# Kernel tuning notes

Hardware: AMD Instinct MI355X
Metric: run time of the kernel (lower is better)

Reference implementation:

```python
import jax, jax.numpy as jnp
import numpy as np

C, H, W = 16, 512, 512
HID = 128
N_STEPS = 8


def setup_inputs() -> dict:
    key = jax.random.key(0)
    k1, k2, k3 = jax.random.split(key, 3)
    state = jax.random.normal(k1, (C, H, W), dtype=jnp.float32)
    # MLP params: 5*C = 80 gathered features -> HID -> C delta channels
    W1 = jax.random.normal(k2, (5 * C, HID), dtype=jnp.float32) * (1.0 / np.sqrt(5 * C))
    b1 = jnp.zeros((HID,), dtype=jnp.float32)
    W2 = jax.random.normal(k3, (HID, C), dtype=jnp.float32) * (1.0 / np.sqrt(HID))
    b2 = jnp.zeros((C,), dtype=jnp.float32)
    return {"state": state, "W1": W1, "b1": b1, "W2": W2, "b2": b2, "n_steps": N_STEPS}


def _neighbor_idx(n):
    i = jnp.arange(n)
    minus = jnp.maximum(i - 1, 0)          # clamp at low edge (cy==0 -> 0)
    plus = jnp.where(i == n - 1, 0, i + 1)  # WRAP to 0 at high edge (original quirk)
    return minus, plus


def reference(state, W1, b1, W2, b2, n_steps):
    c, h, w = state.shape
    up, down = _neighbor_idx(h)
    left, right = _neighbor_idx(w)

    def step(s, _):
        # von-Neumann gather: (5C, H, W), feature order [center, up, down, left, right]
        feats = jnp.concatenate(
            [s, s[:, up, :], s[:, down, :], s[:, :, left], s[:, :, right]], axis=0)
        x = feats.reshape(5 * c, h * w).T        # (HW, 5C)
        hdn = jax.nn.relu(x @ W1 + b1)           # (HW, HID)
        delta = (hdn @ W2 + b2).T.reshape(c, h, w)
        s_new = s + delta
        s_new = s_new.at[0].set(s[0])            # channel 0 snapshot restore
        return s_new, None

    out, _ = jax.lax.scan(step, state, None, length=n_steps)
    return out
```

## Files before the change

### kernel.cpp

```cpp
#include <hip/hip_runtime.h>
#include <hip/hip_bf16.h>

#define HH 512
#define WW 512
#define CC 16
#define HIDN 128
#define HWSZ (HH*WW)

typedef __attribute__((ext_vector_type(8))) short short8;
typedef __attribute__((ext_vector_type(4))) short short4v;
typedef __attribute__((ext_vector_type(4))) float float4v;

__device__ __forceinline__ short to_bf16(float f){
    __hip_bfloat16 h = __float2bfloat16(f);
    return __builtin_bit_cast(short, h);
}

__global__ void __launch_bounds__(256) prep_kernel(
    const float* __restrict__ W1, const float* __restrict__ W2,
    short* __restrict__ w1t, short* __restrict__ w2t)
{
    int t = blockIdx.x * blockDim.x + threadIdx.x;
    int stride = gridDim.x * blockDim.x;
    for (int idx = t; idx < HIDN*96; idx += stride){
        int n = idx / 96;
        int k = idx - n*96;
        float v = (k < 80) ? W1[k*HIDN + n] : 0.0f;
        w1t[idx] = to_bf16(v);
    }
    for (int idx = t; idx < CC*HIDN; idx += stride){
        int n = idx >> 7;
        int k = idx & 127;
        w2t[idx] = to_bf16(W2[k*CC + n]);
    }
}

#define RSTRIDE 24
#define RROW    (68*RSTRIDE)

__global__ void __launch_bounds__(256, 5) step_kernel(
    const float* __restrict__ src, float* __restrict__ dst,
    const short* __restrict__ w1t, const short* __restrict__ w2t,
    const float* __restrict__ b1, const float* __restrict__ b2)
{
    __shared__ __align__(16) short rows_u[3*RROW];
    __shared__ __align__(16) short hdn[64][136];

    const int t    = threadIdx.x;
    const int w    = t >> 6;
    const int lane = t & 63;
    const int ln15 = lane & 15;
    const int g4   = lane >> 4;

    const int bx = blockIdx.x;
    const int y  = bx >> 3;
    const int xs = (bx & 7) << 6;

    const int yu = (y == 0)      ? 0 : (y - 1);
    const int yd = (y == HH - 1) ? 0 : (y + 1);

    if (t < 192){
        const int r  = t >> 6;
        const int l  = t & 63;
        const int q  = l & 15;
        const int cq = l >> 4;
        const int rowg = (r == 0) ? y : ((r == 1) ? yu : yd);
        const float* base = src + (size_t)rowg * WW + xs + (q << 2);
        float4v f[4];
        #pragma unroll
        for (int i = 0; i < 4; ++i)
            f[i] = *(const float4v*)(base + (size_t)((cq << 2) + i) * HWSZ);
        #pragma unroll
        for (int j = 0; j < 4; ++j){
            short4v v;
            v[0] = to_bf16(f[0][j]); v[1] = to_bf16(f[1][j]);
            v[2] = to_bf16(f[2][j]); v[3] = to_bf16(f[3][j]);
            *(short4v*)&rows_u[r*RROW + ((q << 2) + 1 + j)*RSTRIDE + (cq << 2)] = v;
        }
    } else if (t < 224){
        const int c    = (t - 192) & 15;
        const int side = (t - 192) >> 4;
        const int gx   = (side == 0) ? ((xs == 0) ? 0 : xs - 1)
                                     : ((xs + 64 == WW) ? 0 : xs + 64);
        rows_u[(side * 65)*RSTRIDE + c] =
            to_bf16(src[(size_t)c*HWSZ + (size_t)y*WW + gx]);
    }

    int offB[3];
    #pragma unroll
    for (int kk = 0; kk < 3; ++kk){
        const int g  = (kk < 2) ? ((kk << 2) + g4) : (8 + (g4 & 1));
        const int n  = g >> 1;
        const int cb = (g & 1) << 3;
        const int r  = (n == 1) ? 1 : ((n == 2) ? 2 : 0);
        const int dx = (n == 3) ? -1 : ((n == 4) ? 1 : 0);
        offB[kk] = r*RROW + (ln15 + 1 + dx)*RSTRIDE + cb;
    }

    __syncthreads();

    float4v acc[2][4];
    #pragma unroll
    for (int mt = 0; mt < 2; ++mt)
        #pragma unroll
        for (int nt = 0; nt < 4; ++nt)
            acc[mt][nt] = (float4v){0.f, 0.f, 0.f, 0.f};

    #pragma unroll
    for (int kk = 0; kk < 3; ++kk){
        short8 bfragF[4];
        #pragma unroll
        for (int nt = 0; nt < 4; ++nt)
            bfragF[nt] = *(const short8*)(&rows_u[offB[kk] + nt * (16 * RSTRIDE)]);
        #pragma unroll
        for (int mt = 0; mt < 2; ++mt){
            const int hrow = (((w << 1) + mt) << 4) + ln15;
            short8 afragW = *(const short8*)(w1t + hrow * 96 + (kk << 5) + (g4 << 3));
            #pragma unroll
            for (int nt = 0; nt < 4; ++nt)
                acc[mt][nt] = __builtin_amdgcn_mfma_f32_16x16x32_bf16(
                    afragW, bfragF[nt], acc[mt][nt], 0, 0, 0);
        }
    }

    #pragma unroll
    for (int mt = 0; mt < 2; ++mt){
        const int hbase = (((w << 1) + mt) << 4) + (g4 << 2);
        const float4v bb = *(const float4v*)(b1 + hbase);
        #pragma unroll
        for (int nt = 0; nt < 4; ++nt){
            short4v s;
            #pragma unroll
            for (int r = 0; r < 4; ++r){
                float v = acc[mt][nt][r] + bb[r];
                v = v > 0.f ? v : 0.f;
                s[r] = to_bf16(v);
            }
            *(short4v*)&hdn[(nt << 4) + ln15][hbase] = s;
        }
    }
    __syncthreads();

    const int pxb = (w << 4) + (g4 << 2);
    const size_t gofs = (size_t)ln15 * HWSZ + (size_t)y * WW + xs + pxb;
    const float4v sold = *(const float4v*)(src + gofs);
    const float bias2 = b2[ln15];

    float4v acc2 = (float4v){0.f, 0.f, 0.f, 0.f};
    #pragma unroll
    for (int kk = 0; kk < 4; ++kk){
        const int k0 = kk << 5;
        short8 a = *(const short8*)(&hdn[(w << 4) + ln15][k0 + (g4 << 3)]);
        short8 b = *(const short8*)(w2t + ln15 * HIDN + k0 + (g4 << 3));
        acc2 = __builtin_amdgcn_mfma_f32_16x16x32_bf16(a, b, acc2, 0, 0, 0);
    }

    float4v outv;
    #pragma unroll
    for (int r = 0; r < 4; ++r){
        const float v = sold[r] + acc2[r] + bias2;
        outv[r] = (ln15 == 0) ? sold[r] : v;
    }
    *(float4v*)(dst + gofs) = outv;
}

extern "C" void kernel_launch(void* const* d_in, const int* in_sizes, int n_in,
                              void* d_out, int out_size, void* d_ws, size_t ws_size,
                              hipStream_t stream)
{
    const float* state = (const float*)d_in[0];
    const float* W1    = (const float*)d_in[1];
    const float* b1    = (const float*)d_in[2];
    const float* W2    = (const float*)d_in[3];
    const float* b2    = (const float*)d_in[4];

    float* B1  = (float*)d_ws;
    short* w1t = (short*)((char*)d_ws + (size_t)HWSZ * CC * 4);
    short* w2t = w1t + HIDN * 96;
    float* out = (float*)d_out;

    prep_kernel<<<32, 256, 0, stream>>>(W1, W2, w1t, w2t);

    dim3 grid(HH * (WW / 64));
    step_kernel<<<grid, 256, 0, stream>>>(state, B1, w1t, w2t, b1, b2);
    step_kernel<<<grid, 256, 0, stream>>>(B1, out, w1t, w2t, b1, b2);
    step_kernel<<<grid, 256, 0, stream>>>(out, B1, w1t, w2t, b1, b2);
    step_kernel<<<grid, 256, 0, stream>>>(B1, out, w1t, w2t, b1, b2);
    step_kernel<<<grid, 256, 0, stream>>>(out, B1, w1t, w2t, b1, b2);
    step_kernel<<<grid, 256, 0, stream>>>(B1, out, w1t, w2t, b1, b2);
    step_kernel<<<grid, 256, 0, stream>>>(out, B1, w1t, w2t, b1, b2);
    step_kernel<<<grid, 256, 0, stream>>>(B1, out, w1t, w2t, b1, b2);
}
```

Baseline: 264.2 us.

## Fuse eight step launches into one persistent cooperative kernel with grid sync

Replaces the eight per-step kernel launches with a single cooperative kernel of 1024 blocks. Each block processes four strips per step, and a grid-wide barrier separates consecutive steps, which removes launch gaps and per-launch tail effects. If the cooperative launch fails, it falls back to the original eight launches. The trade-off is grid-sync overhead, a lower occupancy bound (4 blocks per SM instead of 5), and a missing __syncthreads between strips that reuse the same shared buffers, which risks a race.

```diff
diff --git a/kernel.cpp b/kernel.cpp
--- a/kernel.cpp
+++ b/kernel.cpp
@@ -1,5 +1,8 @@
 #include <hip/hip_runtime.h>
 #include <hip/hip_bf16.h>
+#include <hip/hip_cooperative_groups.h>
+
+namespace cg = cooperative_groups;
 
 #define HH 512
 #define WW 512
@@ -38,24 +41,13 @@
 #define RSTRIDE 24
 #define RROW    (68*RSTRIDE)
 
-__global__ void __launch_bounds__(256, 5) step_kernel(
+__device__ __forceinline__ void do_strip(
     const float* __restrict__ src, float* __restrict__ dst,
     const short* __restrict__ w1t, const short* __restrict__ w2t,
-    const float* __restrict__ b1, const float* __restrict__ b2)
-{
-    __shared__ __align__(16) short rows_u[3*RROW];
-    __shared__ __align__(16) short hdn[64][136];
-
-    const int t    = threadIdx.x;
-    const int w    = t >> 6;
-    const int lane = t & 63;
-    const int ln15 = lane & 15;
-    const int g4   = lane >> 4;
-
-    const int bx = blockIdx.x;
-    const int y  = bx >> 3;
-    const int xs = (bx & 7) << 6;
-
+    const float* __restrict__ b1, const float bias2,
+    short* __restrict__ rows_u, short (*hdn)[136], const int* offB,
+    int t, int w, int ln15, int g4, int y, int xs)
+{
     const int yu = (y == 0)      ? 0 : (y - 1);
     const int yd = (y == HH - 1) ? 0 : (y + 1);
 
@@ -85,18 +77,6 @@
         rows_u[(side * 65)*RSTRIDE + c] =
             to_bf16(src[(size_t)c*HWSZ + (size_t)y*WW + gx]);
     }
-
-    int offB[3];
-    #pragma unroll
-    for (int kk = 0; kk < 3; ++kk){
-        const int g  = (kk < 2) ? ((kk << 2) + g4) : (8 + (g4 & 1));
-        const int n  = g >> 1;
-        const int cb = (g & 1) << 3;
-        const int r  = (n == 1) ? 1 : ((n == 2) ? 2 : 0);
-        const int dx = (n == 3) ? -1 : ((n == 4) ? 1 : 0);
-        offB[kk] = r*RROW + (ln15 + 1 + dx)*RSTRIDE + cb;
-    }
-
     __syncthreads();
 
     float4v acc[2][4];
@@ -144,7 +124,6 @@
     const int pxb = (w << 4) + (g4 << 2);
     const size_t gofs = (size_t)ln15 * HWSZ + (size_t)y * WW + xs + pxb;
     const float4v sold = *(const float4v*)(src + gofs);
-    const float bias2 = b2[ln15];
 
     float4v acc2 = (float4v){0.f, 0.f, 0.f, 0.f};
     #pragma unroll
@@ -164,15 +143,95 @@
     *(float4v*)(dst + gofs) = outv;
 }
 
+__global__ void __launch_bounds__(256, 4) fused_kernel(
+    const float* __restrict__ state, float* __restrict__ B1, float* __restrict__ out,
+    const short* __restrict__ w1t, const short* __restrict__ w2t,
+    const float* __restrict__ b1, const float* __restrict__ b2)
+{
+    cg::grid_group gg = cg::this_grid();
+
+    __shared__ __align__(16) short rows_u[3*RROW];
+    __shared__ __align__(16) short hdn[64][136];
+
+    const int t    = threadIdx.x;
+    const int w    = t >> 6;
+    const int lane = t & 63;
+    const int ln15 = lane & 15;
+    const int g4   = lane >> 4;
+    const int b    = blockIdx.x;
+
+    int offB[3];
+    #pragma unroll
+    for (int kk = 0; kk < 3; ++kk){
+        const int g  = (kk < 2) ? ((kk << 2) + g4) : (8 + (g4 & 1));
+        const int n  = g >> 1;
+        const int cb = (g & 1) << 3;
+        const int r  = (n == 1) ? 1 : ((n == 2) ? 2 : 0);
+        const int dx = (n == 3) ? -1 : ((n == 4) ? 1 : 0);
+        offB[kk] = r*RROW + (ln15 + 1 + dx)*RSTRIDE + cb;
+    }
+    const float bias2 = b2[ln15];
+
+    #pragma unroll 1
+    for (int step = 0; step < 8; ++step){
+        const float* src = (step == 0) ? state : ((step & 1) ? B1 : out);
+        float* dst = (step & 1) ? out : B1;
+
+        #pragma unroll 1
+        for (int i = 0; i < 4; ++i){
+            const int s  = b + (i << 10);
+            const int y  = s >> 3;
+            const int xs = (s & 7) << 6;
+            do_strip(src, dst, w1t, w2t, b1, bias2,
+                     rows_u, hdn, offB, t, w, ln15, g4, y, xs);
+        }
+        if (step < 7) gg.sync();
+    }
+}
+
+__global__ void __launch_bounds__(256, 5) step_kernel(
+    const float* __restrict__ src, float* __restrict__ dst,
+    const short* __restrict__ w1t, const short* __restrict__ w2t,
+    const float* __restrict__ b1, const float* __restrict__ b2)
+{
+    __shared__ __align__(16) short rows_u[3*RROW];
+    __shared__ __align__(16) short hdn[64][136];
+
+    const int t    = threadIdx.x;
+    const int w    = t >> 6;
+    const int lane = t & 63;
+    const int ln15 = lane & 15;
+    const int g4   = lane >> 4;
+
+    const int bx = blockIdx.x;
+    const int y  = bx >> 3;
+    const int xs = (bx & 7) << 6;
+
+    int offB[3];
+    #pragma unroll
+    for (int kk = 0; kk < 3; ++kk){
+        const int g  = (kk < 2) ? ((kk << 2) + g4) : (8 + (g4 & 1));
+        const int n  = g >> 1;
+        const int cb = (g & 1) << 3;
+        const int r  = (n == 1) ? 1 : ((n == 2) ? 2 : 0);
+        const int dx = (n == 3) ? -1 : ((n == 4) ? 1 : 0);
+        offB[kk] = r*RROW + (ln15 + 1 + dx)*RSTRIDE + cb;
+    }
+    const float bias2 = b2[ln15];
+
+    do_strip(src, dst, w1t, w2t, b1, bias2,
+             rows_u, hdn, offB, t, w, ln15, g4, y, xs);
+}
+
 extern "C" void kernel_launch(void* const* d_in, const int* in_sizes, int n_in,
                               void* d_out, int out_size, void* d_ws, size_t ws_size,
                               hipStream_t stream)
 {
     const float* state = (const float*)d_in[0];
     const float* W1    = (const float*)d_in[1];
-    const float* b1    = (const float*)d_in[2];
+    const float* b1p   = (const float*)d_in[2];
     const float* W2    = (const float*)d_in[3];
-    const float* b2    = (const float*)d_in[4];
+    const float* b2p   = (const float*)d_in[4];
 
     float* B1  = (float*)d_ws;
     short* w1t = (short*)((char*)d_ws + (size_t)HWSZ * CC * 4);
@@ -181,13 +240,23 @@
 
     prep_kernel<<<32, 256, 0, stream>>>(W1, W2, w1t, w2t);
 
-    dim3 grid(HH * (WW / 64));
-    step_kernel<<<grid, 256, 0, stream>>>(state, B1, w1t, w2t, b1, b2);
-    step_kernel<<<grid, 256, 0, stream>>>(B1, out, w1t, w2t, b1, b2);
-    step_kernel<<<grid, 256, 0, stream>>>(out, B1, w1t, w2t, b1, b2);
-    step_kernel<<<grid, 256, 0, stream>>>(B1, out, w1t, w2t, b1, b2);
-    step_kernel<<<grid, 256, 0, stream>>>(out, B1, w1t, w2t, b1, b2);
-    step_kernel<<<grid, 256, 0, stream>>>(B1, out, w1t, w2t, b1, b2);
-    step_kernel<<<grid, 256, 0, stream>>>(out, B1, w1t, w2t, b1, b2);
-    step_kernel<<<grid, 256, 0, stream>>>(B1, out, w1t, w2t, b1, b2);
-}
+    void* kargs[] = {
+        (void*)&state, (void*)&B1, (void*)&out,
+        (void*)&w1t, (void*)&w2t, (void*)&b1p, (void*)&b2p
+    };
+    hipError_t err = hipLaunchCooperativeKernel(
+        (const void*)fused_kernel, dim3(1024), dim3(256), kargs, 0, stream);
+
+    if (err != hipSuccess){
+        (void)hipGetLastError();
+        dim3 grid(HH * (WW / 64));
+        step_kernel<<<grid, 256, 0, stream>>>(state, B1, w1t, w2t, b1p, b2p);
+        step_kernel<<<grid, 256, 0, stream>>>(B1, out, w1t, w2t, b1p, b2p);
+        step_kernel<<<grid, 256, 0, stream>>>(out, B1, w1t, w2t, b1p, b2p);
+        step_kernel<<<grid, 256, 0, stream>>>(B1, out, w1t, w2t, b1p, b2p);
+        step_kernel<<<grid, 256, 0, stream>>>(out, B1, w1t, w2t, b1p, b2p);
+        step_kernel<<<grid, 256, 0, stream>>>(B1, out, w1t, w2t, b1p, b2p);
+        step_kernel<<<grid, 256, 0, stream>>>(out, B1, w1t, w2t, b1p, b2p);
+        step_kernel<<<grid, 256, 0, stream>>>(B1, out, w1t, w2t, b1p, b2p);
+    }
+}
```

Measured after the change: 1.025 ms. 288% more time.

## Fuse two automaton steps per kernel with halo recomputation of neighbor rows

Applied to the files above, without the earlier changes.

Each kernel launch now performs two update steps. The block recomputes the first step for its own row and the rows above and below (plus a 1-pixel column halo) into shared memory, then computes the second step from those values. This halves the number of launches and global round-trips of the state, at the cost of roughly three times the first-step MLP work, more shared memory and lower occupancy.

```diff
diff --git a/kernel.cpp b/kernel.cpp
--- a/kernel.cpp
+++ b/kernel.cpp
@@ -10,6 +10,7 @@
 typedef __attribute__((ext_vector_type(8))) short short8;
 typedef __attribute__((ext_vector_type(4))) short short4v;
 typedef __attribute__((ext_vector_type(4))) float float4v;
+typedef __attribute__((ext_vector_type(2))) float float2v;
 
 __device__ __forceinline__ short to_bf16(float f){
     __hip_bfloat16 h = __float2bfloat16(f);
@@ -38,13 +39,15 @@
 #define RSTRIDE 24
 #define RROW    (68*RSTRIDE)
 
-__global__ void __launch_bounds__(256, 5) step_kernel(
+__global__ void __launch_bounds__(256, 4) step2_kernel(
     const float* __restrict__ src, float* __restrict__ dst,
     const short* __restrict__ w1t, const short* __restrict__ w2t,
     const float* __restrict__ b1, const float* __restrict__ b2)
 {
+    __shared__ __align__(16) short rows_s[3*RROW];
     __shared__ __align__(16) short rows_u[3*RROW];
-    __shared__ __align__(16) short hdn[64][136];
+    __shared__ __align__(16) short hdn[66][136];
+    float* ctr = (float*)rows_s;
 
     const int t    = threadIdx.x;
     const int w    = t >> 6;
@@ -59,34 +62,7 @@
     const int yu = (y == 0)      ? 0 : (y - 1);
     const int yd = (y == HH - 1) ? 0 : (y + 1);
 
-    if (t < 192){
-        const int r  = t >> 6;
-        const int l  = t & 63;
-        const int q  = l & 15;
-        const int cq = l >> 4;
-        const int rowg = (r == 0) ? y : ((r == 1) ? yu : yd);
-        const float* base = src + (size_t)rowg * WW + xs + (q << 2);
-        float4v f[4];
-        #pragma unroll
-        for (int i = 0; i < 4; ++i)
-            f[i] = *(const float4v*)(base + (size_t)((cq << 2) + i) * HWSZ);
-        #pragma unroll
-        for (int j = 0; j < 4; ++j){
-            short4v v;
-            v[0] = to_bf16(f[0][j]); v[1] = to_bf16(f[1][j]);
-            v[2] = to_bf16(f[2][j]); v[3] = to_bf16(f[3][j]);
-            *(short4v*)&rows_u[r*RROW + ((q << 2) + 1 + j)*RSTRIDE + (cq << 2)] = v;
-        }
-    } else if (t < 224){
-        const int c    = (t - 192) & 15;
-        const int side = (t - 192) >> 4;
-        const int gx   = (side == 0) ? ((xs == 0) ? 0 : xs - 1)
-                                     : ((xs + 64 == WW) ? 0 : xs + 64);
-        rows_u[(side * 65)*RSTRIDE + c] =
-            to_bf16(src[(size_t)c*HWSZ + (size_t)y*WW + gx]);
-    }
-
-    int offB[3];
+    int offA[3];
     #pragma unroll
     for (int kk = 0; kk < 3; ++kk){
         const int g  = (kk < 2) ? ((kk << 2) + g4) : (8 + (g4 & 1));
@@ -94,74 +70,199 @@
         const int cb = (g & 1) << 3;
         const int r  = (n == 1) ? 1 : ((n == 2) ? 2 : 0);
         const int dx = (n == 3) ? -1 : ((n == 4) ? 1 : 0);
-        offB[kk] = r*RROW + (ln15 + 1 + dx)*RSTRIDE + cb;
-    }
-
+        offA[kk] = r*RROW + (ln15 + 1 + dx)*RSTRIDE + cb;
+    }
+    const float bias2 = b2[ln15];
+
+    const int excA = (xs == 0   && ln15 == 0) ? RSTRIDE : 0;
+    const int excB = (xs == 448 && ln15 == 1 && g4 >= 2) ? RSTRIDE : 0;
+
+    #pragma unroll 1
+    for (int pass = 0; pass < 3; ++pass){
+        const int slot = (pass == 0) ? 1 : ((pass == 1) ? 2 : 0);
+        const int gr   = (pass == 0) ? yu : ((pass == 1) ? yd : y);
+
+        if (t < 204){
+            const int r3 = (t >= 136) ? 2 : ((t >= 68) ? 1 : 0);
+            const int u  = t - r3 * 68;
+            const int q  = u >> 2;
+            const int cq = u & 3;
+            const int rowg = (r3 == 0) ? gr
+                           : ((r3 == 1) ? ((gr == 0) ? 0 : gr - 1)
+                                        : ((gr == HH - 1) ? 0 : gr + 1));
+            const int c0 = xs - 2 + (q << 2);
+            float4v f[4];
+            if (c0 >= 0 && c0 <= 508){
+                const float* base = src + (size_t)rowg * WW + c0;
+                #pragma unroll
+                for (int i = 0; i < 4; ++i){
+                    const float* p = base + (size_t)((cq << 2) + i) * HWSZ;
+                    float2v lo = *(const float2v*)(p);
+                    float2v hi = *(const float2v*)(p + 2);
+                    f[i][0] = lo[0]; f[i][1] = lo[1]; f[i][2] = hi[0]; f[i][3] = hi[1];
+                }
+            } else {
+                #pragma unroll
+                for (int j = 0; j < 4; ++j){
+                    int c = c0 + j;
+                    c = (c < 0) ? 0 : ((c >= 512) ? c - 512 : c);
+                    #pragma unroll
+                    for (int i = 0; i < 4; ++i)
+                        f[i][j] = src[(size_t)((cq << 2) + i) * HWSZ + (size_t)rowg * WW + c];
+                }
+            }
+            #pragma unroll
+            for (int j = 0; j < 4; ++j){
+                short4v v;
+                v[0] = to_bf16(f[0][j]); v[1] = to_bf16(f[1][j]);
+                v[2] = to_bf16(f[2][j]); v[3] = to_bf16(f[3][j]);
+                *(short4v*)&rows_s[r3*RROW + ((q << 2) + j)*RSTRIDE + (cq << 2)] = v;
+            }
+        }
+        __syncthreads();
+
+        float4v acc[2][5];
+        #pragma unroll
+        for (int mt = 0; mt < 2; ++mt)
+            #pragma unroll
+            for (int nt = 0; nt < 5; ++nt)
+                acc[mt][nt] = (float4v){0.f, 0.f, 0.f, 0.f};
+
+        #pragma unroll
+        for (int kk = 0; kk < 3; ++kk){
+            short8 bfragF[5];
+            #pragma unroll
+            for (int nt = 0; nt < 5; ++nt){
+                int ao = offA[kk] + nt * (16 * RSTRIDE);
+                if (kk == 2 && nt == 0) ao += excA;
+                if (kk == 1 && nt == 4) ao += excB;
+                bfragF[nt] = *(const short8*)(&rows_s[ao]);
+            }
+            #pragma unroll
+            for (int mt = 0; mt < 2; ++mt){
+                const int hrow = (((w << 1) + mt) << 4) + ln15;
+                short8 afragW = *(const short8*)(w1t + hrow * 96 + (kk << 5) + (g4 << 3));
+                #pragma unroll
+                for (int nt = 0; nt < 5; ++nt)
+                    acc[mt][nt] = __builtin_amdgcn_mfma_f32_16x16x32_bf16(
+                        afragW, bfragF[nt], acc[mt][nt], 0, 0, 0);
+            }
+        }
+
+        #pragma unroll
+        for (int mt = 0; mt < 2; ++mt){
+            const int hbase = (((w << 1) + mt) << 4) + (g4 << 2);
+            const float4v bb = *(const float4v*)(b1 + hbase);
+            #pragma unroll
+            for (int nt = 0; nt < 5; ++nt){
+                if (nt == 4 && ln15 >= 2) continue;
+                short4v s;
+                #pragma unroll
+                for (int r = 0; r < 4; ++r){
+                    float v = acc[mt][nt][r] + bb[r];
+                    v = v > 0.f ? v : 0.f;
+                    s[r] = to_bf16(v);
+                }
+                *(short4v*)&hdn[(nt << 4) + ln15][hbase] = s;
+            }
+        }
+        __syncthreads();
+
+        #pragma unroll 1
+        for (int tile = w; tile < 5; tile += 4){
+            const int arow = (tile < 4) ? ((tile << 4) + ln15) : (64 + (ln15 & 1));
+            float4v a2 = (float4v){0.f, 0.f, 0.f, 0.f};
+            #pragma unroll
+            for (int kk = 0; kk < 4; ++kk){
+                const int k0 = kk << 5;
+                short8 a = *(const short8*)(&hdn[arow][k0 + (g4 << 3)]);
+                short8 b = *(const short8*)(w2t + ln15 * HIDN + k0 + (g4 << 3));
+                a2 = __builtin_amdgcn_mfma_f32_16x16x32_bf16(a, b, a2, 0, 0, 0);
+            }
+            const int pb = (tile << 4) + (g4 << 2);
+            #pragma unroll
+            for (int r = 0; r < 4; ++r){
+                const int p = pb + r;
+                int c = xs - 1 + p;
+                c = (c < 0) ? 0 : ((c >= 512) ? c - 512 : c);
+                const float sold = src[(size_t)ln15 * HWSZ + (size_t)gr * WW + c];
+                const float val = (ln15 == 0) ? sold : (sold + a2[r] + bias2);
+                if (p <= 65){
+                    rows_u[slot * RROW + p * RSTRIDE + ln15] = to_bf16(val);
+                    if (slot == 0 && p >= 1 && p <= 64)
+                        ctr[((p - 1) << 4) + ln15] = val;
+                }
+            }
+        }
+    }
     __syncthreads();
 
-    float4v acc[2][4];
-    #pragma unroll
-    for (int mt = 0; mt < 2; ++mt)
-        #pragma unroll
-        for (int nt = 0; nt < 4; ++nt)
-            acc[mt][nt] = (float4v){0.f, 0.f, 0.f, 0.f};
-
-    #pragma unroll
-    for (int kk = 0; kk < 3; ++kk){
-        short8 bfragF[4];
-        #pragma unroll
-        for (int nt = 0; nt < 4; ++nt)
-            bfragF[nt] = *(const short8*)(&rows_u[offB[kk] + nt * (16 * RSTRIDE)]);
+    {
+        float4v acc[2][4];
+        #pragma unroll
+        for (int mt = 0; mt < 2; ++mt)
+            #pragma unroll
+            for (int nt = 0; nt < 4; ++nt)
+                acc[mt][nt] = (float4v){0.f, 0.f, 0.f, 0.f};
+
+        #pragma unroll
+        for (int kk = 0; kk < 3; ++kk){
+            short8 bfragF[4];
+            #pragma unroll
+            for (int nt = 0; nt < 4; ++nt)
+                bfragF[nt] = *(const short8*)(&rows_u[offA[kk] + nt * (16 * RSTRIDE)]);
+            #pragma unroll
+            for (int mt = 0; mt < 2; ++mt){
+                const int hrow = (((w << 1) + mt) << 4) + ln15;
+                short8 afragW = *(const short8*)(w1t + hrow * 96 + (kk << 5) + (g4 << 3));
+                #pragma unroll
+                for (int nt = 0; nt < 4; ++nt)
+                    acc[mt][nt] = __builtin_amdgcn_mfma_f32_16x16x32_bf16(
+                        afragW, bfragF[nt], acc[mt][nt], 0, 0, 0);
+            }
+        }
+
         #pragma unroll
         for (int mt = 0; mt < 2; ++mt){
-            const int hrow = (((w << 1) + mt) << 4) + ln15;
-            short8 afragW = *(const short8*)(w1t + hrow * 96 + (kk << 5) + (g4 << 3));
-            #pragma unroll
-            for (int nt = 0; nt < 4; ++nt)
-                acc[mt][nt] = __builtin_amdgcn_mfma_f32_16x16x32_bf16(
-                    afragW, bfragF[nt], acc[mt][nt], 0, 0, 0);
-        }
-    }
-
-    #pragma unroll
-    for (int mt = 0; mt < 2; ++mt){
-        const int hbase = (((w << 1) + mt) << 4) + (g4 << 2);
-        const float4v bb = *(const float4v*)(b1 + hbase);
-        #pragma unroll
-        for (int nt = 0; nt < 4; ++nt){
-            short4v s;
-            #pragma unroll
-            for (int r = 0; r < 4; ++r){
-                float v = acc[mt][nt][r] + bb[r];
-                v = v > 0.f ? v : 0.f;
-                s[r] = to_bf16(v);
-            }
-            *(short4v*)&hdn[(nt << 4) + ln15][hbase] = s;
+            const int hbase = (((w << 1) + mt) << 4) + (g4 << 2);
+            const float4v bb = *(const float4v*)(b1 + hbase);
+            #pragma unroll
+            for (int nt = 0; nt < 4; ++nt){
+                short4v s;
+                #pragma unroll
+                for (int r = 0; r < 4; ++r){
+                    float v = acc[mt][nt][r] + bb[r];
+                    v = v > 0.f ? v : 0.f;
+                    s[r] = to_bf16(v);
+                }
+                *(short4v*)&hdn[(nt << 4) + ln15][hbase] = s;
+            }
         }
     }
     __syncthreads();
 
-    const int pxb = (w << 4) + (g4 << 2);
-    const size_t gofs = (size_t)ln15 * HWSZ + (size_t)y * WW + xs + pxb;
-    const float4v sold = *(const float4v*)(src + gofs);
-    const float bias2 = b2[ln15];
-
-    float4v acc2 = (float4v){0.f, 0.f, 0.f, 0.f};
-    #pragma unroll
-    for (int kk = 0; kk < 4; ++kk){
-        const int k0 = kk << 5;
-        short8 a = *(const short8*)(&hdn[(w << 4) + ln15][k0 + (g4 << 3)]);
-        short8 b = *(const short8*)(w2t + ln15 * HIDN + k0 + (g4 << 3));
-        acc2 = __builtin_amdgcn_mfma_f32_16x16x32_bf16(a, b, acc2, 0, 0, 0);
-    }
-
-    float4v outv;
-    #pragma unroll
-    for (int r = 0; r < 4; ++r){
-        const float v = sold[r] + acc2[r] + bias2;
-        outv[r] = (ln15 == 0) ? sold[r] : v;
-    }
-    *(float4v*)(dst + gofs) = outv;
+    {
+        const int pxb = (w << 4) + (g4 << 2);
+        const size_t gofs = (size_t)ln15 * HWSZ + (size_t)y * WW + xs + pxb;
+
+        float4v a2 = (float4v){0.f, 0.f, 0.f, 0.f};
+        #pragma unroll
+        for (int kk = 0; kk < 4; ++kk){
+            const int k0 = kk << 5;
+            short8 a = *(const short8*)(&hdn[(w << 4) + ln15][k0 + (g4 << 3)]);
+            short8 b = *(const short8*)(w2t + ln15 * HIDN + k0 + (g4 << 3));
+            a2 = __builtin_amdgcn_mfma_f32_16x16x32_bf16(a, b, a2, 0, 0, 0);
+        }
+
+        float4v outv;
+        #pragma unroll
+        for (int r = 0; r < 4; ++r){
+            const float sold = ctr[((pxb + r) << 4) + ln15];
+            const float v = sold + a2[r] + bias2;
+            outv[r] = (ln15 == 0) ? sold : v;
+        }
+        *(float4v*)(dst + gofs) = outv;
+    }
 }
 
 extern "C" void kernel_launch(void* const* d_in, const int* in_sizes, int n_in,
@@ -170,9 +271,9 @@
 {
     const float* state = (const float*)d_in[0];
     const float* W1    = (const float*)d_in[1];
-    const float* b1    = (const float*)d_in[2];
+    const float* b1p   = (const float*)d_in[2];
     const float* W2    = (const float*)d_in[3];
-    const float* b2    = (const float*)d_in[4];
+    const float* b2p   = (const float*)d_in[4];
 
     float* B1  = (float*)d_ws;
     short* w1t = (short*)((char*)d_ws + (size_t)HWSZ * CC * 4);
@@ -182,12 +283,8 @@
     prep_kernel<<<32, 256, 0, stream>>>(W1, W2, w1t, w2t);
 
     dim3 grid(HH * (WW / 64));
-    step_kernel<<<grid, 256, 0, stream>>>(state, B1, w1t, w2t, b1, b2);
-    step_kernel<<<grid, 256, 0, stream>>>(B1, out, w1t, w2t, b1, b2);
-    step_kernel<<<grid, 256, 0, stream>>>(out, B1, w1t, w2t, b1, b2);
-    step_kernel<<<grid, 256, 0, stream>>>(B1, out, w1t, w2t, b1, b2);
-    step_kernel<<<grid, 256, 0, stream>>>(out, B1, w1t, w2t, b1, b2);
-    step_kernel<<<grid, 256, 0, stream>>>(B1, out, w1t, w2t, b1, b2);
-    step_kernel<<<grid, 256, 0, stream>>>(out, B1, w1t, w2t, b1, b2);
-    step_kernel<<<grid, 256, 0, stream>>>(B1, out, w1t, w2t, b1, b2);
-}
+    step2_kernel<<<grid, 256, 0, stream>>>(state, B1, w1t, w2t, b1p, b2p);
+    step2_kernel<<<grid, 256, 0, stream>>>(B1, out, w1t, w2t, b1p, b2p);
+    step2_kernel<<<grid, 256, 0, stream>>>(out, B1, w1t, w2t, b1p, b2p);
+    step2_kernel<<<grid, 256, 0, stream>>>(B1, out, w1t, w2t, b1p, b2p);
+}
```

After: 559.0 us. 112% more time.

## Process four tiles per block with register prefetch of next tile

Applied to the files above, without the earlier changes.

Each block now handles four consecutive 64-pixel tiles along a row instead of one. The grid shrinks from 4096 to 1024 blocks, and block indices are remapped so blocks are interleaved across rows. The next tile's global loads are issued into registers before the current tile's MFMA work, so load latency overlaps compute. The aim is to cut per-block launch and setup overhead and hide memory latency. The cost is fewer blocks, which lowers available parallelism, and extra live registers for the prefetch.

```diff
diff --git a/kernel.cpp b/kernel.cpp
--- a/kernel.cpp
+++ b/kernel.cpp
@@ -38,27 +38,10 @@
 #define RSTRIDE 24
 #define RROW    (68*RSTRIDE)
 
-__global__ void __launch_bounds__(256, 5) step_kernel(
-    const float* __restrict__ src, float* __restrict__ dst,
-    const short* __restrict__ w1t, const short* __restrict__ w2t,
-    const float* __restrict__ b1, const float* __restrict__ b2)
-{
-    __shared__ __align__(16) short rows_u[3*RROW];
-    __shared__ __align__(16) short hdn[64][136];
-
-    const int t    = threadIdx.x;
-    const int w    = t >> 6;
-    const int lane = t & 63;
-    const int ln15 = lane & 15;
-    const int g4   = lane >> 4;
-
-    const int bx = blockIdx.x;
-    const int y  = bx >> 3;
-    const int xs = (bx & 7) << 6;
-
-    const int yu = (y == 0)      ? 0 : (y - 1);
-    const int yd = (y == HH - 1) ? 0 : (y + 1);
-
+__device__ __forceinline__ void stage_load(
+    const float* __restrict__ src, int t, int y, int yu, int yd, int xs,
+    float4v f[4], float* halo)
+{
     if (t < 192){
         const int r  = t >> 6;
         const int l  = t & 63;
@@ -66,10 +49,26 @@
         const int cq = l >> 4;
         const int rowg = (r == 0) ? y : ((r == 1) ? yu : yd);
         const float* base = src + (size_t)rowg * WW + xs + (q << 2);
-        float4v f[4];
         #pragma unroll
         for (int i = 0; i < 4; ++i)
             f[i] = *(const float4v*)(base + (size_t)((cq << 2) + i) * HWSZ);
+    } else if (t < 224){
+        const int c    = (t - 192) & 15;
+        const int side = (t - 192) >> 4;
+        const int gx   = (side == 0) ? ((xs == 0) ? 0 : xs - 1)
+                                     : ((xs + 64 == WW) ? 0 : xs + 64);
+        *halo = src[(size_t)c * HWSZ + (size_t)y * WW + gx];
+    }
+}
+
+__device__ __forceinline__ void stage_write(
+    short* __restrict__ rows_u, int t, const float4v f[4], float halo)
+{
+    if (t < 192){
+        const int r  = t >> 6;
+        const int l  = t & 63;
+        const int q  = l & 15;
+        const int cq = l >> 4;
         #pragma unroll
         for (int j = 0; j < 4; ++j){
             short4v v;
@@ -80,11 +79,31 @@
     } else if (t < 224){
         const int c    = (t - 192) & 15;
         const int side = (t - 192) >> 4;
-        const int gx   = (side == 0) ? ((xs == 0) ? 0 : xs - 1)
-                                     : ((xs + 64 == WW) ? 0 : xs + 64);
-        rows_u[(side * 65)*RSTRIDE + c] =
-            to_bf16(src[(size_t)c*HWSZ + (size_t)y*WW + gx]);
-    }
+        rows_u[(side * 65)*RSTRIDE + c] = to_bf16(halo);
+    }
+}
+
+__global__ void __launch_bounds__(256, 5) step_kernel(
+    const float* __restrict__ src, float* __restrict__ dst,
+    const short* __restrict__ w1t, const short* __restrict__ w2t,
+    const float* __restrict__ b1, const float* __restrict__ b2)
+{
+    __shared__ __align__(16) short rows_u[3*RROW];
+    __shared__ __align__(16) short hdn[64][136];
+
+    const int t    = threadIdx.x;
+    const int w    = t >> 6;
+    const int lane = t & 63;
+    const int ln15 = lane & 15;
+    const int g4   = lane >> 4;
+
+    const int b  = blockIdx.x;
+    const int vb = ((b & 7) << 7) | (b >> 3);
+    const int y  = vb >> 1;
+    const int xs0 = ((vb & 1) << 2) << 6;
+
+    const int yu = (y == 0)      ? 0 : (y - 1);
+    const int yd = (y == HH - 1) ? 0 : (y + 1);
 
     int offB[3];
     #pragma unroll
@@ -96,72 +115,85 @@
         const int dx = (n == 3) ? -1 : ((n == 4) ? 1 : 0);
         offB[kk] = r*RROW + (ln15 + 1 + dx)*RSTRIDE + cb;
     }
-
-    __syncthreads();
-
-    float4v acc[2][4];
-    #pragma unroll
-    for (int mt = 0; mt < 2; ++mt)
-        #pragma unroll
-        for (int nt = 0; nt < 4; ++nt)
-            acc[mt][nt] = (float4v){0.f, 0.f, 0.f, 0.f};
-
-    #pragma unroll
-    for (int kk = 0; kk < 3; ++kk){
-        short8 bfragF[4];
-        #pragma unroll
-        for (int nt = 0; nt < 4; ++nt)
-            bfragF[nt] = *(const short8*)(&rows_u[offB[kk] + nt * (16 * RSTRIDE)]);
+    const float bias2 = b2[ln15];
+
+    float4v pf[4];
+    float   ph = 0.f;
+    stage_load(src, t, y, yu, yd, xs0, pf, &ph);
+
+    #pragma unroll 1
+    for (int u = 0; u < 4; ++u){
+        const int xs = xs0 + (u << 6);
+
+        stage_write(rows_u, t, pf, ph);
+        __syncthreads();
+
+        if (u < 3)
+            stage_load(src, t, y, yu, yd, xs + 64, pf, &ph);
+
+        const int pxb = (w << 4) + (g4 << 2);
+        const size_t gofs = (size_t)ln15 * HWSZ + (size_t)y * WW + xs + pxb;
+        const float4v sold = *(const float4v*)(src + gofs);
+
+        float4v acc[2][4];
+        #pragma unroll
+        for (int mt = 0; mt < 2; ++mt)
+            #pragma unroll
+            for (int nt = 0; nt < 4; ++nt)
+                acc[mt][nt] = (float4v){0.f, 0.f, 0.f, 0.f};
+
+        #pragma unroll
+        for (int kk = 0; kk < 3; ++kk){
+            short8 bfragF[4];
+            #pragma unroll
+            for (int nt = 0; nt < 4; ++nt)
+                bfragF[nt] = *(const short8*)(&rows_u[offB[kk] + nt * (16 * RSTRIDE)]);
+            #pragma unroll
+            for (int mt = 0; mt < 2; ++mt){
+                const int hrow = (((w << 1) + mt) << 4) + ln15;
+                short8 afragW = *(const short8*)(w1t + hrow * 96 + (kk << 5) + (g4 << 3));
+                #pragma unroll
+                for (int nt = 0; nt < 4; ++nt)
+                    acc[mt][nt] = __builtin_amdgcn_mfma_f32_16x16x32_bf16(
+                        afragW, bfragF[nt], acc[mt][nt], 0, 0, 0);
+            }
+        }
+
         #pragma unroll
         for (int mt = 0; mt < 2; ++mt){
-            const int hrow = (((w << 1) + mt) << 4) + ln15;
-            short8 afragW = *(const short8*)(w1t + hrow * 96 + (kk << 5) + (g4 << 3));
-            #pragma unroll
-            for (int nt = 0; nt < 4; ++nt)
-                acc[mt][nt] = __builtin_amdgcn_mfma_f32_16x16x32_bf16(
-                    afragW, bfragF[nt], acc[mt][nt], 0, 0, 0);
-        }
-    }
-
-    #pragma unroll
-    for (int mt = 0; mt < 2; ++mt){
-        const int hbase = (((w << 1) + mt) << 4) + (g4 << 2);
-        const float4v bb = *(const float4v*)(b1 + hbase);
-        #pragma unroll
-        for (int nt = 0; nt < 4; ++nt){
-            short4v s;
-            #pragma unroll
-            for (int r = 0; r < 4; ++r){
-                float v = acc[mt][nt][r] + bb[r];
-                v = v > 0.f ? v : 0.f;
-                s[r] = to_bf16(v);
+            const int hbase = (((w << 1) + mt) << 4) + (g4 << 2);
+            const float4v bb = *(const float4v*)(b1 + hbase);
+            #pragma unroll
+            for (int nt = 0; nt < 4; ++nt){
+                short4v s;
+                #pragma unroll
+                for (int r = 0; r < 4; ++r){
+                    float v = acc[mt][nt][r] + bb[r];
+                    v = v > 0.f ? v : 0.f;
+                    s[r] = to_bf16(v);
+                }
+                *(short4v*)&hdn[(nt << 4) + ln15][hbase] = s;
             }
-            *(short4v*)&hdn[(nt << 4) + ln15][hbase] = s;
-        }
-    }
-    __syncthreads();
-
-    const int pxb = (w << 4) + (g4 << 2);
-    const size_t gofs = (size_t)ln15 * HWSZ + (size_t)y * WW + xs + pxb;
-    const float4v sold = *(const float4v*)(src + gofs);
-    const float bias2 = b2[ln15];
-
-    float4v acc2 = (float4v){0.f, 0.f, 0.f, 0.f};
-    #pragma unroll
-    for (int kk = 0; kk < 4; ++kk){
-        const int k0 = kk << 5;
-        short8 a = *(const short8*)(&hdn[(w << 4) + ln15][k0 + (g4 << 3)]);
-        short8 b = *(const short8*)(w2t + ln15 * HIDN + k0 + (g4 << 3));
-        acc2 = __builtin_amdgcn_mfma_f32_16x16x32_bf16(a, b, acc2, 0, 0, 0);
-    }
-
-    float4v outv;
-    #pragma unroll
-    for (int r = 0; r < 4; ++r){
-        const float v = sold[r] + acc2[r] + bias2;
-        outv[r] = (ln15 == 0) ? sold[r] : v;
-    }
-    *(float4v*)(dst + gofs) = outv;
+        }
+        __syncthreads();
+
+        float4v acc2 = (float4v){0.f, 0.f, 0.f, 0.f};
+        #pragma unroll
+        for (int kk = 0; kk < 4; ++kk){
+            const int k0 = kk << 5;
+            short8 a = *(const short8*)(&hdn[(w << 4) + ln15][k0 + (g4 << 3)]);
+            short8 bfr = *(const short8*)(w2t + ln15 * HIDN + k0 + (g4 << 3));
+            acc2 = __builtin_amdgcn_mfma_f32_16x16x32_bf16(a, bfr, acc2, 0, 0, 0);
+        }
+
+        float4v outv;
+        #pragma unroll
+        for (int r = 0; r < 4; ++r){
+            const float v = sold[r] + acc2[r] + bias2;
+            outv[r] = (ln15 == 0) ? sold[r] : v;
+        }
+        *(float4v*)(dst + gofs) = outv;
+    }
 }
 
 extern "C" void kernel_launch(void* const* d_in, const int* in_sizes, int n_in,
@@ -170,9 +202,9 @@
 {
     const float* state = (const float*)d_in[0];
     const float* W1    = (const float*)d_in[1];
-    const float* b1    = (const float*)d_in[2];
+    const float* b1p   = (const float*)d_in[2];
     const float* W2    = (const float*)d_in[3];
-    const float* b2    = (const float*)d_in[4];
+    const float* b2p   = (const float*)d_in[4];
 
     float* B1  = (float*)d_ws;
     short* w1t = (short*)((char*)d_ws + (size_t)HWSZ * CC * 4);
@@ -181,13 +213,13 @@
 
     prep_kernel<<<32, 256, 0, stream>>>(W1, W2, w1t, w2t);
 
-    dim3 grid(HH * (WW / 64));
-    step_kernel<<<grid, 256, 0, stream>>>(state, B1, w1t, w2t, b1, b2);
-    step_kernel<<<grid, 256, 0, stream>>>(B1, out, w1t, w2t, b1, b2);
-    step_kernel<<<grid, 256, 0, stream>>>(out, B1, w1t, w2t, b1, b2);
-    step_kernel<<<grid, 256, 0, stream>>>(B1, out, w1t, w2t, b1, b2);
-    step_kernel<<<grid, 256, 0, stream>>>(out, B1, w1t, w2t, b1, b2);
-    step_kernel<<<grid, 256, 0, stream>>>(B1, out, w1t, w2t, b1, b2);
-    step_kernel<<<grid, 256, 0, stream>>>(out, B1, w1t, w2t, b1, b2);
-    step_kernel<<<grid, 256, 0, stream>>>(B1, out, w1t, w2t, b1, b2);
-}
+    dim3 grid(1024);
+    step_kernel<<<grid, 256, 0, stream>>>(state, B1, w1t, w2t, b1p, b2p);
+    step_kernel<<<grid, 256, 0, stream>>>(B1, out, w1t, w2t, b1p, b2p);
+    step_kernel<<<grid, 256, 0, stream>>>(out, B1, w1t, w2t, b1p, b2p);
+    step_kernel<<<grid, 256, 0, stream>>>(B1, out, w1t, w2t, b1p, b2p);
+    step_kernel<<<grid, 256, 0, stream>>>(out, B1, w1t, w2t, b1p, b2p);
+    step_kernel<<<grid, 256, 0, stream>>>(B1, out, w1t, w2t, b1p, b2p);
+    step_kernel<<<grid, 256, 0, stream>>>(out, B1, w1t, w2t, b1p, b2p);
+    step_kernel<<<grid, 256, 0, stream>>>(B1, out, w1t, w2t, b1p, b2p);
+}
```

Result: slower. 329.7 us (+24.8%).
